# Performance work log

Hardware: AMD Instinct MI355X
Metric: run time of the kernel (lower is better)

The kernel has to match this reference:

```python
import jax, jax.numpy as jnp
import numpy as np

B, S, V, E, HID = 16, 40, 1004, 256, 256
C, R, HW = 1024, 256, 32  # featureChannel, releMapChannel, spatial
BN_EPS = 1e-5


def setup_inputs() -> dict:
    key = jax.random.key(0)
    ks = jax.random.split(key, 16)
    sc = 0.05
    emb = jax.random.normal(ks[4], (V, E), jnp.float32) * sc
    emb = emb.at[0].set(0.0)  # padding_idx = 0
    return {
        "feature": jax.random.normal(ks[0], (B, C, HW, HW), jnp.float32),
        "depth": jax.random.uniform(ks[1], (B, 1, HW, HW), jnp.float32),
        "instruction_idx": jax.random.randint(ks[2], (B, S), 0, V, jnp.int32),
        "instruction_length": jnp.clip(jax.random.randint(ks[3], (B,), 1, S + 1, jnp.int32), 1, S),
        "only_train_rele": 1,
        "emb_table": emb,
        "w_ih": jax.random.normal(ks[5], (4 * HID, E), jnp.float32) * sc,
        "w_hh": jax.random.normal(ks[6], (4 * HID, HID), jnp.float32) * sc,
        "b_ih": jax.random.normal(ks[7], (4 * HID,), jnp.float32) * sc,
        "b_hh": jax.random.normal(ks[8], (4 * HID,), jnp.float32) * sc,
        "e2d_w": jax.random.normal(ks[9], (HID, HID), jnp.float32) * sc,
        "e2d_b": jax.random.normal(ks[10], (HID,), jnp.float32) * sc,
        "lin1_w": jax.random.normal(ks[11], (R * C, HID), jnp.float32) * sc,
        "lin1_b": jax.random.normal(ks[12], (R * C,), jnp.float32) * sc,
        "bn_gamma": jnp.ones((R,), jnp.float32),
        "bn_beta": jnp.zeros((R,), jnp.float32),
        "bn_mean": jax.random.normal(ks[13], (R,), jnp.float32) * 0.01,
        "bn_var": jnp.ones((R,), jnp.float32),
    }


def _encoder_lstm(idx, lengths, emb_table, w_ih, w_hh, b_ih, b_hh, e2d_w, e2d_b):
    # Faithful to packed-sequence LSTM: state stops updating at each sample's length.
    embeds = emb_table[idx]                      # [B,S,E]
    xs = jnp.swapaxes(embeds, 0, 1)              # [S,B,E]
    mask = (jnp.arange(S)[:, None] < lengths[None, :])  # [S,B]
    h0 = jnp.zeros((B, HID), embeds.dtype)
    c0 = jnp.zeros((B, HID), embeds.dtype)

    def step(carry, xm):
        h, c = carry
        x_t, m = xm                              # [B,E], [B]
        gates = x_t @ w_ih.T + h @ w_hh.T + (b_ih + b_hh)  # [B,4H]
        i, f, g, o = jnp.split(gates, 4, axis=-1)  # torch gate order: i,f,g,o
        c_new = jax.nn.sigmoid(f) * c + jax.nn.sigmoid(i) * jnp.tanh(g)
        h_new = jax.nn.sigmoid(o) * jnp.tanh(c_new)
        m = m[:, None]
        return (jnp.where(m, h_new, h), jnp.where(m, c_new, c)), None

    (h_t, _), _ = jax.lax.scan(step, (h0, c0), (xs, mask))
    return jnp.tanh(h_t @ e2d_w.T + e2d_b)       # [B,HID]


def reference(feature, depth, instruction_idx, instruction_length, only_train_rele,
              emb_table, w_ih, w_hh, b_ih, b_hh, e2d_w, e2d_b,
              lin1_w, lin1_b, bn_gamma, bn_beta, bn_mean, bn_var):
    instr = _encoder_lstm(instruction_idx, instruction_length, emb_table,
                          w_ih, w_hh, b_ih, b_hh, e2d_w, e2d_b)  # [B,HID]
    # per-sample dynamic 1x1 filters (dropout in eval mode -> identity)
    f1 = jax.nn.leaky_relu(instr @ lin1_w.T + lin1_b, negative_slope=0.01)
    f1 = f1.reshape(B, R, C)
    # batched per-sample 1x1 conv: one einsum replaces the batch loop of F.conv2d
    rele = jax.nn.relu(jnp.einsum('bchw,brc->brhw', feature, f1))  # [B,R,H,W]
    # BatchNorm2d in eval mode with running stats
    scale = bn_gamma / jnp.sqrt(bn_var + BN_EPS)
    rele = rele * scale[None, :, None, None] + (bn_beta - bn_mean * scale)[None, :, None, None]
    single = jnp.max(rele, axis=1)               # channel-max pooling -> [B,H,W]
    return jnp.clip(single, 0.0, 1.0)
```

## Files before the change

kernel.cpp:

```cpp
#include <hip/hip_runtime.h>
#include <hip/hip_fp16.h>
#include <math.h>

#define NB 16
#define SQ 40
#define HIDN 256
#define CC 1024
#define NROW 262144

#define AGENT __HIP_MEMORY_SCOPE_AGENT
#define SENT 0x7E7E7E7Eu

__device__ __forceinline__ float sigf(float x){ return 1.0f/(1.0f+__expf(-x)); }

typedef _Float16 h2v __attribute__((ext_vector_type(2)));
typedef _Float16 f16x8 __attribute__((ext_vector_type(8)));
typedef float    f32x4 __attribute__((ext_vector_type(4)));

__device__ __forceinline__ float fd2(unsigned w, unsigned h, float acc){
  h2v a = __builtin_bit_cast(h2v, w);
  h2v b = __builtin_bit_cast(h2v, h);
#if __has_builtin(__builtin_amdgcn_fdot2)
  return __builtin_amdgcn_fdot2(a, b, acc, false);
#else
  return acc + (float)a.x*(float)b.x + (float)a.y*(float)b.y;
#endif
}

__device__ __forceinline__ unsigned pkh(float lo, float hi){
  return (unsigned)__half_as_ushort(__float2half_rn(lo))
       | ((unsigned)__half_as_ushort(__float2half_rn(hi)) << 16);
}

__global__ __launch_bounds__(256) void k_xgates(
    const int* __restrict__ idx, const float* __restrict__ emb,
    const float* __restrict__ w_ih, const float* __restrict__ b_ih,
    const float* __restrict__ b_hh, float* __restrict__ XG)
{
  __shared__ float xs[8*256];
  int t = threadIdx.x;
  int tb0 = blockIdx.x * 8;
  #pragma unroll
  for (int i = 0; i < 8; ++i) {
    int flat = t + i*256;
    int p = flat >> 8, k = flat & 255;
    int tb = tb0 + p;
    int ts = tb >> 4, b = tb & 15;
    int row = idx[b*SQ + ts];
    xs[p*256 + k] = emb[row*256 + k];
  }
  __syncthreads();
  int rows[4];
  float acc[4][8];
  #pragma unroll
  for (int r = 0; r < 4; ++r) {
    rows[r] = t + r*256;
    float bias = b_ih[rows[r]] + b_hh[rows[r]];
    #pragma unroll
    for (int p = 0; p < 8; ++p) acc[r][p] = bias;
  }
  for (int k16 = 0; k16 < 16; ++k16) {
    float4 w[4][4];
    #pragma unroll
    for (int r = 0; r < 4; ++r)
      #pragma unroll
      for (int q = 0; q < 4; ++q)
        w[r][q] = *(const float4*)&w_ih[rows[r]*256 + k16*16 + q*4];
    #pragma unroll
    for (int p = 0; p < 8; ++p) {
      #pragma unroll
      for (int q = 0; q < 4; ++q) {
        float4 x = *(const float4*)&xs[p*256 + k16*16 + q*4];
        #pragma unroll
        for (int r = 0; r < 4; ++r)
          acc[r][p] += w[r][q].x*x.x + w[r][q].y*x.y + w[r][q].z*x.z + w[r][q].w*x.w;
      }
    }
  }
  #pragma unroll
  for (int p = 0; p < 8; ++p)
    #pragma unroll
    for (int r = 0; r < 4; ++r)
      XG[(tb0 + p)*1024 + rows[r]] = acc[r][p];
}

__global__ __launch_bounds__(256) void k_whh3(const float* __restrict__ w, unsigned* __restrict__ W3)
{
  int tid = blockIdx.x*256 + threadIdx.x;
  int c    = tid & 3;
  int tt   = (tid >> 2) & 511;
  int q    = (tid >> 11) & 31;
  int half = tid >> 16;
  int pair = 4*q + c;
  int g = tt >> 7, j = tt & 127;
  int row = g*256 + half*128 + j;
  float2 v = *(const float2*)&w[(size_t)row*256 + 2*pair];
  W3[tid] = pkh(v.x, v.y);
}

__global__ __launch_bounds__(512) void k_lstm2(
    const float* __restrict__ XG, const uint4* __restrict__ W3,
    const int* __restrict__ lens, const float* __restrict__ e2d_w,
    const float* __restrict__ e2d_b, float* __restrict__ instr,
    unsigned* __restrict__ hcomm)
{
  __shared__ float dot_s[512];
  __shared__ float h_s[128];
  __shared__ float h_e[256];

  int t = threadIdx.x;
  int b    = blockIdx.x & 15;
  int half = blockIdx.x >> 4;
  int len  = lens[b];
  int lane = t & 63;

  unsigned wv[128];
  {
    const uint4* wp = W3 + (size_t)half*32*512 + t;
    #pragma unroll
    for (int q = 0; q < 32; ++q) {
      uint4 v = wp[(size_t)q*512];
      wv[4*q+0]=v.x; wv[4*q+1]=v.y; wv[4*q+2]=v.z; wv[4*q+3]=v.w;
    }
  }

  int g = t >> 7, j = t & 127;
  int row = g*256 + half*128 + j;
  float c_reg = 0.0f, h_reg = 0.0f;

  for (int it = 0; it < SQ; ++it) {
    float acc = XG[(it*NB + b)*1024 + row];
    if (it > 0) {
      unsigned own = pkh(h_s[2*lane], h_s[2*lane + 1]);
      int owni = (int)own;
      const unsigned* oslot = hcomm + ((it-1)*NB + b)*128 + (half ? 0 : 64);
      if (half == 0) {
        #pragma unroll
        for (int q = 0; q < 64; ++q)
          acc = fd2(wv[q], (unsigned)__builtin_amdgcn_readlane(owni, q), acc);
        unsigned oth;
        do { oth = __hip_atomic_load(oslot + lane, __ATOMIC_RELAXED, AGENT); }
        while (__any((int)(oth == SENT)));
        int othi = (int)oth;
        #pragma unroll
        for (int q = 0; q < 64; ++q)
          acc = fd2(wv[64+q], (unsigned)__builtin_amdgcn_readlane(othi, q), acc);
      } else {
        #pragma unroll
        for (int q = 0; q < 64; ++q)
          acc = fd2(wv[64+q], (unsigned)__builtin_amdgcn_readlane(owni, q), acc);
        unsigned oth;
        do { oth = __hip_atomic_load(oslot + lane, __ATOMIC_RELAXED, AGENT); }
        while (__any((int)(oth == SENT)));
        int othi = (int)oth;
        #pragma unroll
        for (int q = 0; q < 64; ++q)
          acc = fd2(wv[q], (unsigned)__builtin_amdgcn_readlane(othi, q), acc);
      }
    }
    dot_s[t] = acc;
    __syncthreads();
    if (t < 128) {
      float iv = sigf (dot_s[t]);
      float fv = sigf (dot_s[t + 128]);
      float gv = tanhf(dot_s[t + 256]);
      float ov = sigf (dot_s[t + 384]);
      float cn = fv*c_reg + iv*gv;
      float hn = ov*tanhf(cn);
      if (it < len) { c_reg = cn; h_reg = hn; }
      h_s[t] = h_reg;
    }
    __syncthreads();
    if (t < 64)
      __hip_atomic_store(hcomm + (it*NB + b)*128 + half*64 + t,
                         pkh(h_s[2*t], h_s[2*t+1]), __ATOMIC_RELAXED, AGENT);
  }

  if (half == 0) {
    const unsigned* slot = hcomm + ((SQ-1)*NB + b)*128;
    if (t < 64) {
      unsigned v0, v1;
      do {
        v0 = __hip_atomic_load(slot + t,      __ATOMIC_RELAXED, AGENT);
        v1 = __hip_atomic_load(slot + 64 + t, __ATOMIC_RELAXED, AGENT);
      } while (__any((int)(v0 == SENT)) || __any((int)(v1 == SENT)));
      h2v lo = __builtin_bit_cast(h2v, v0);
      h2v hi = __builtin_bit_cast(h2v, v1);
      h_e[2*t]       = (float)lo.x;  h_e[2*t + 1]       = (float)lo.y;
      h_e[128 + 2*t] = (float)hi.x;  h_e[128 + 2*t + 1] = (float)hi.y;
    }
    __syncthreads();
    if (t < 256) {
      float acc2 = e2d_b[t];
      const float4* wp2 = (const float4*)&e2d_w[t*256];
      #pragma unroll 8
      for (int k4 = 0; k4 < 64; ++k4) {
        float4 w = wp2[k4];
        float4 h4 = *(const float4*)&h_e[k4*4];
        acc2 += w.x*h4.x + w.y*h4.y + w.z*h4.z + w.w*h4.w;
      }
      instr[b*256 + t] = tanhf(acc2);
    }
  }
}

__global__ __launch_bounds__(256) void k_lin1(
    const float* __restrict__ instr, const float* __restrict__ w,
    const float* __restrict__ bias, _Float16* __restrict__ f1h)
{
  __shared__ float is[4096];
  int t = threadIdx.x;
  #pragma unroll
  for (int i = 0; i < 16; ++i) is[t + i*256] = instr[t + i*256];
  __syncthreads();
  int r0 = blockIdx.x*512 + t;
  int r1 = r0 + 256;
  const float* w0 = &w[(size_t)r0*256];
  const float* w1 = &w[(size_t)r1*256];
  float acc0[16], acc1[16];
  float bz0 = bias[r0], bz1 = bias[r1];
  #pragma unroll
  for (int i = 0; i < 16; ++i){ acc0[i]=bz0; acc1[i]=bz1; }
  for (int k16 = 0; k16 < 16; ++k16) {
    float4 a[4], bb[4];
    #pragma unroll
    for (int q = 0; q < 4; ++q){
      a[q]  = *(const float4*)&w0[k16*16 + q*4];
      bb[q] = *(const float4*)&w1[k16*16 + q*4];
    }
    #pragma unroll
    for (int bi = 0; bi < 16; ++bi) {
      #pragma unroll
      for (int q = 0; q < 4; ++q) {
        float4 x = *(const float4*)&is[bi*256 + k16*16 + q*4];
        acc0[bi] += a[q].x*x.x + a[q].y*x.y + a[q].z*x.z + a[q].w*x.w;
        acc1[bi] += bb[q].x*x.x + bb[q].y*x.y + bb[q].z*x.z + bb[q].w*x.w;
      }
    }
  }
  #pragma unroll
  for (int bi = 0; bi < 16; ++bi) {
    float v0 = acc0[bi]; v0 = v0 > 0.0f ? v0 : 0.01f*v0;
    float v1 = acc1[bi]; v1 = v1 > 0.0f ? v1 : 0.01f*v1;
    f1h[(size_t)bi*NROW + r0] = (_Float16)v0;
    f1h[(size_t)bi*NROW + r1] = (_Float16)v1;
  }
}

__global__ __launch_bounds__(256, 1) void k_einsum_mfma(
    const uint4* __restrict__ f1h4, const float* __restrict__ feat,
    const float* __restrict__ gamma, const float* __restrict__ beta,
    const float* __restrict__ mean, const float* __restrict__ var,
    float* __restrict__ out)
{
  __shared__ unsigned ALDS[256*20];
  __shared__ unsigned BLDS[128*20];
  __shared__ float sc_s[256], sh_s[256];
  __shared__ float red[2][128];

  int t = threadIdx.x;
  int b  = blockIdx.x >> 3;
  int P0 = (blockIdx.x & 7) * 128;
  int wid  = t >> 6, lane = t & 63;
  int wp = wid & 1, wr = wid >> 1;
  int col = lane & 15, quad = lane >> 4;

  {
    float s = gamma[t] * rsqrtf(var[t] + 1e-5f);
    sc_s[t] = s;
    sh_s[t] = beta[t] - mean[t]*s;
  }

  f32x4 acc[8][4];
  #pragma unroll
  for (int mt = 0; mt < 8; ++mt)
    #pragma unroll
    for (int nt = 0; nt < 4; ++nt) acc[mt][nt] = (f32x4)0.0f;

  const uint4* arow = f1h4 + ((size_t)b*NROW + (size_t)t*1024)/8;
  int p_loc = t & 127, khalf = t >> 7;
  const float* bbase = feat + ((size_t)b*1024 + khalf*16)*1024 + P0 + p_loc;

  uint4 apf[4];
  float bpf[16];
  #pragma unroll
  for (int g = 0; g < 4; ++g) apf[g] = arow[g];
  #pragma unroll
  for (int j = 0; j < 16; ++j) bpf[j] = bbase[(size_t)j*1024];

  for (int kc = 0; kc < 32; ++kc) {
    __syncthreads();
    #pragma unroll
    for (int g = 0; g < 4; ++g)
      *(uint4*)&ALDS[t*20 + g*4] = apf[g];
    {
      unsigned u[8];
      #pragma unroll
      for (int i = 0; i < 8; ++i) u[i] = pkh(bpf[2*i], bpf[2*i+1]);
      uint4 w0 = {u[0],u[1],u[2],u[3]}, w1 = {u[4],u[5],u[6],u[7]};
      *(uint4*)&BLDS[p_loc*20 + khalf*8]     = w0;
      *(uint4*)&BLDS[p_loc*20 + khalf*8 + 4] = w1;
    }
    __syncthreads();
    if (kc + 1 < 32) {
      #pragma unroll
      for (int g = 0; g < 4; ++g) apf[g] = arow[(kc+1)*4 + g];
      const float* bb = bbase + (size_t)(kc+1)*32*1024;
      #pragma unroll
      for (int j = 0; j < 16; ++j) bpf[j] = bb[(size_t)j*1024];
    }
    f16x8 bf[4];
    #pragma unroll
    for (int nt = 0; nt < 4; ++nt) {
      uint4 raw = *(const uint4*)&BLDS[(wp*64 + nt*16 + col)*20 + quad*4];
      bf[nt] = __builtin_bit_cast(f16x8, raw);
    }
    #pragma unroll
    for (int mt = 0; mt < 8; ++mt) {
      uint4 raw = *(const uint4*)&ALDS[(wr*128 + mt*16 + col)*20 + quad*4];
      f16x8 af = __builtin_bit_cast(f16x8, raw);
      #pragma unroll
      for (int nt = 0; nt < 4; ++nt)
        acc[mt][nt] = __builtin_amdgcn_mfma_f32_16x16x32_f16(af, bf[nt], acc[mt][nt], 0, 0, 0);
    }
  }

  float pmax[4];
  #pragma unroll
  for (int nt = 0; nt < 4; ++nt) pmax[nt] = -3.4e38f;
  #pragma unroll
  for (int mt = 0; mt < 8; ++mt) {
    int rb = wr*128 + mt*16 + quad*4;
    f32x4 scv = *(const f32x4*)&sc_s[rb];
    f32x4 shv = *(const f32x4*)&sh_s[rb];
    #pragma unroll
    for (int nt = 0; nt < 4; ++nt) {
      f32x4 a = acc[mt][nt];
      #pragma unroll
      for (int reg = 0; reg < 4; ++reg) {
        float v = fmaxf(a[reg], 0.0f)*scv[reg] + shv[reg];
        pmax[nt] = fmaxf(pmax[nt], v);
      }
    }
  }
  #pragma unroll
  for (int nt = 0; nt < 4; ++nt) {
    float m = pmax[nt];
    m = fmaxf(m, __shfl_xor(m, 16));
    m = fmaxf(m, __shfl_xor(m, 32));
    if (lane < 16) red[wr][wp*64 + nt*16 + lane] = m;
  }
  __syncthreads();
  if (t < 128) {
    float v = fmaxf(red[0][t], red[1][t]);
    out[b*1024 + P0 + t] = fminf(fmaxf(v, 0.0f), 1.0f);
  }
}

extern "C" void kernel_launch(void* const* d_in, const int* in_sizes, int n_in,
                              void* d_out, int out_size, void* d_ws, size_t ws_size,
                              hipStream_t stream)
{
  const float* feature = (const float*)d_in[0];
  const int*   idx     = (const int*)d_in[2];
  const int*   lens    = (const int*)d_in[3];
  const float* emb     = (const float*)d_in[5];
  const float* w_ih    = (const float*)d_in[6];
  const float* w_hh    = (const float*)d_in[7];
  const float* b_ih    = (const float*)d_in[8];
  const float* b_hh    = (const float*)d_in[9];
  const float* e2d_w   = (const float*)d_in[10];
  const float* e2d_b   = (const float*)d_in[11];
  const float* lin1_w  = (const float*)d_in[12];
  const float* lin1_b  = (const float*)d_in[13];
  const float* gamma   = (const float*)d_in[14];
  const float* beta    = (const float*)d_in[15];
  const float* mean    = (const float*)d_in[16];
  const float* var     = (const float*)d_in[17];

  char* ws = (char*)d_ws;
  float*    XG     = (float*)(ws);
  float*    instr  = (float*)(ws + 2621440);
  unsigned* W3     = (unsigned*)(ws + 2637824);
  unsigned* hcomm  = (unsigned*)(ws + 3162112);
  _Float16* f1h    = (_Float16*)(ws + 3489792);

  hipMemsetAsync(hcomm, 0x7E, 327680, stream);
  k_xgates <<<80,  256, 0, stream>>>(idx, emb, w_ih, b_ih, b_hh, XG);
  k_whh3   <<<512, 256, 0, stream>>>(w_hh, W3);
  k_lstm2  <<<32,  512, 0, stream>>>(XG, (const uint4*)W3, lens, e2d_w, e2d_b, instr, hcomm);
  k_lin1   <<<512, 256, 0, stream>>>(instr, lin1_w, lin1_b, f1h);
  k_einsum_mfma <<<128, 256, 0, stream>>>((const uint4*)f1h, feature, gamma, beta, mean, var,
                                          (float*)d_out);
}
```

Before: 614.7 us.

## Use one 1024-thread LSTM block per sample and double grid sizes of lin1/einsum

Replaces the two-block-per-sample LSTM, which exchanged hidden state through global atomics with spin-waits and a memset, with a single 1024-thread block per sample. Each thread now holds one full row of W_hh in fp16 registers, and the hidden state is shared through LDS. The next step's XG value is prefetched and the dot product is split into two accumulators to shorten the dependency chain. The lin1 kernel drops from two rows per thread to one, and the einsum tile shrinks from 128 to 64 pixels per block. Both grids double, giving more parallelism at the cost of more redundant A-tile loads in the einsum.

Result: slower. 1.184 ms (+92.6%).

```diff
diff --git a/kernel.cpp b/kernel.cpp
--- a/kernel.cpp
+++ b/kernel.cpp
@@ -7,9 +7,6 @@
 #define HIDN 256
 #define CC 1024
 #define NROW 262144
-
-#define AGENT __HIP_MEMORY_SCOPE_AGENT
-#define SENT 0x7E7E7E7Eu
 
 __device__ __forceinline__ float sigf(float x){ return 1.0f/(1.0f+__expf(-x)); }
 
@@ -84,123 +81,100 @@
       XG[(tb0 + p)*1024 + rows[r]] = acc[r][p];
 }
 
-__global__ __launch_bounds__(256) void k_whh3(const float* __restrict__ w, unsigned* __restrict__ W3)
+__global__ __launch_bounds__(256) void k_whh4(const float* __restrict__ w, uint4* __restrict__ W4)
 {
   int tid = blockIdx.x*256 + threadIdx.x;
-  int c    = tid & 3;
-  int tt   = (tid >> 2) & 511;
-  int q    = (tid >> 11) & 31;
-  int half = tid >> 16;
-  int pair = 4*q + c;
-  int g = tt >> 7, j = tt & 127;
-  int row = g*256 + half*128 + j;
-  float2 v = *(const float2*)&w[(size_t)row*256 + 2*pair];
-  W3[tid] = pkh(v.x, v.y);
-}
-
-__global__ __launch_bounds__(512) void k_lstm2(
-    const float* __restrict__ XG, const uint4* __restrict__ W3,
+  int row = tid >> 5;
+  int q4  = tid & 31;
+  const float* src = &w[(size_t)row*256 + q4*8];
+  float4 a = *(const float4*)src;
+  float4 b = *(const float4*)(src + 4);
+  uint4 o;
+  o.x = pkh(a.x, a.y);
+  o.y = pkh(a.z, a.w);
+  o.z = pkh(b.x, b.y);
+  o.w = pkh(b.z, b.w);
+  W4[(size_t)q4*1024 + row] = o;
+}
+
+__global__ __launch_bounds__(1024) void k_lstm1b(
+    const float* __restrict__ XG, const uint4* __restrict__ W4,
     const int* __restrict__ lens, const float* __restrict__ e2d_w,
-    const float* __restrict__ e2d_b, float* __restrict__ instr,
-    unsigned* __restrict__ hcomm)
-{
-  __shared__ float dot_s[512];
-  __shared__ float h_s[128];
-  __shared__ float h_e[256];
+    const float* __restrict__ e2d_b, float* __restrict__ instr)
+{
+  __shared__ float dot_s[1024];
+  __shared__ float h_s[256];
+  __shared__ unsigned h_pk[128];
 
   int t = threadIdx.x;
-  int b    = blockIdx.x & 15;
-  int half = blockIdx.x >> 4;
-  int len  = lens[b];
+  int b = blockIdx.x;
+  int len = lens[b];
   int lane = t & 63;
 
   unsigned wv[128];
+  #pragma unroll
+  for (int q4 = 0; q4 < 32; ++q4) {
+    uint4 v = W4[(size_t)q4*1024 + t];
+    wv[4*q4+0]=v.x; wv[4*q4+1]=v.y; wv[4*q4+2]=v.z; wv[4*q4+3]=v.w;
+  }
+
+  float c0 = 0.0f, c1 = 0.0f, h0r = 0.0f, h1r = 0.0f;
+
+  float xg_cur = XG[(0*NB + b)*1024 + t];
+
+  for (int it = 0; it < SQ; ++it) {
+    float xg_next = (it+1 < SQ) ? XG[((it+1)*NB + b)*1024 + t] : 0.0f;
+    float acc = xg_cur;
+    if (it > 0) {
+      int hp0 = (int)h_pk[lane];
+      int hp1 = (int)h_pk[64 + lane];
+      float a0 = acc, a1 = 0.0f;
+      #pragma unroll
+      for (int q = 0; q < 64; q += 2) {
+        a0 = fd2(wv[q],   (unsigned)__builtin_amdgcn_readlane(hp0, q),   a0);
+        a1 = fd2(wv[q+1], (unsigned)__builtin_amdgcn_readlane(hp0, q+1), a1);
+      }
+      #pragma unroll
+      for (int q = 0; q < 64; q += 2) {
+        a0 = fd2(wv[64+q],   (unsigned)__builtin_amdgcn_readlane(hp1, q),   a0);
+        a1 = fd2(wv[64+q+1], (unsigned)__builtin_amdgcn_readlane(hp1, q+1), a1);
+      }
+      acc = a0 + a1;
+    }
+    dot_s[t] = acc;
+    __syncthreads();
+    if (t < 128) {
+      float2 di = *(const float2*)&dot_s[2*t];
+      float2 df = *(const float2*)&dot_s[2*t + 256];
+      float2 dg = *(const float2*)&dot_s[2*t + 512];
+      float2 dv = *(const float2*)&dot_s[2*t + 768];
+      float cn0 = sigf(df.x)*c0 + sigf(di.x)*tanhf(dg.x);
+      float hn0 = sigf(dv.x)*tanhf(cn0);
+      float cn1 = sigf(df.y)*c1 + sigf(di.y)*tanhf(dg.y);
+      float hn1 = sigf(dv.y)*tanhf(cn1);
+      if (it < len) { c0 = cn0; h0r = hn0; c1 = cn1; h1r = hn1; }
+      h_pk[t] = pkh(h0r, h1r);
+      h_s[2*t] = h0r; h_s[2*t + 1] = h1r;
+    }
+    __syncthreads();
+    xg_cur = xg_next;
+  }
+
   {
-    const uint4* wp = W3 + (size_t)half*32*512 + t;
-    #pragma unroll
-    for (int q = 0; q < 32; ++q) {
-      uint4 v = wp[(size_t)q*512];
-      wv[4*q+0]=v.x; wv[4*q+1]=v.y; wv[4*q+2]=v.z; wv[4*q+3]=v.w;
-    }
-  }
-
-  int g = t >> 7, j = t & 127;
-  int row = g*256 + half*128 + j;
-  float c_reg = 0.0f, h_reg = 0.0f;
-
-  for (int it = 0; it < SQ; ++it) {
-    float acc = XG[(it*NB + b)*1024 + row];
-    if (it > 0) {
-      unsigned own = pkh(h_s[2*lane], h_s[2*lane + 1]);
-      int owni = (int)own;
-      const unsigned* oslot = hcomm + ((it-1)*NB + b)*128 + (half ? 0 : 64);
-      if (half == 0) {
-        #pragma unroll
-        for (int q = 0; q < 64; ++q)
-          acc = fd2(wv[q], (unsigned)__builtin_amdgcn_readlane(owni, q), acc);
-        unsigned oth;
-        do { oth = __hip_atomic_load(oslot + lane, __ATOMIC_RELAXED, AGENT); }
-        while (__any((int)(oth == SENT)));
-        int othi = (int)oth;
-        #pragma unroll
-        for (int q = 0; q < 64; ++q)
-          acc = fd2(wv[64+q], (unsigned)__builtin_amdgcn_readlane(othi, q), acc);
-      } else {
-        #pragma unroll
-        for (int q = 0; q < 64; ++q)
-          acc = fd2(wv[64+q], (unsigned)__builtin_amdgcn_readlane(owni, q), acc);
-        unsigned oth;
-        do { oth = __hip_atomic_load(oslot + lane, __ATOMIC_RELAXED, AGENT); }
-        while (__any((int)(oth == SENT)));
-        int othi = (int)oth;
-        #pragma unroll
-        for (int q = 0; q < 64; ++q)
-          acc = fd2(wv[q], (unsigned)__builtin_amdgcn_readlane(othi, q), acc);
-      }
-    }
-    dot_s[t] = acc;
-    __syncthreads();
-    if (t < 128) {
-      float iv = sigf (dot_s[t]);
-      float fv = sigf (dot_s[t + 128]);
-      float gv = tanhf(dot_s[t + 256]);
-      float ov = sigf (dot_s[t + 384]);
-      float cn = fv*c_reg + iv*gv;
-      float hn = ov*tanhf(cn);
-      if (it < len) { c_reg = cn; h_reg = hn; }
-      h_s[t] = h_reg;
-    }
-    __syncthreads();
-    if (t < 64)
-      __hip_atomic_store(hcomm + (it*NB + b)*128 + half*64 + t,
-                         pkh(h_s[2*t], h_s[2*t+1]), __ATOMIC_RELAXED, AGENT);
-  }
-
-  if (half == 0) {
-    const unsigned* slot = hcomm + ((SQ-1)*NB + b)*128;
-    if (t < 64) {
-      unsigned v0, v1;
-      do {
-        v0 = __hip_atomic_load(slot + t,      __ATOMIC_RELAXED, AGENT);
-        v1 = __hip_atomic_load(slot + 64 + t, __ATOMIC_RELAXED, AGENT);
-      } while (__any((int)(v0 == SENT)) || __any((int)(v1 == SENT)));
-      h2v lo = __builtin_bit_cast(h2v, v0);
-      h2v hi = __builtin_bit_cast(h2v, v1);
-      h_e[2*t]       = (float)lo.x;  h_e[2*t + 1]       = (float)lo.y;
-      h_e[128 + 2*t] = (float)hi.x;  h_e[128 + 2*t + 1] = (float)hi.y;
-    }
-    __syncthreads();
-    if (t < 256) {
-      float acc2 = e2d_b[t];
-      const float4* wp2 = (const float4*)&e2d_w[t*256];
-      #pragma unroll 8
-      for (int k4 = 0; k4 < 64; ++k4) {
-        float4 w = wp2[k4];
-        float4 h4 = *(const float4*)&h_e[k4*4];
-        acc2 += w.x*h4.x + w.y*h4.y + w.z*h4.z + w.w*h4.w;
-      }
-      instr[b*256 + t] = tanhf(acc2);
-    }
+    int r2 = t & 255, g2 = t >> 8;
+    float part = 0.0f;
+    const float4* wp2 = (const float4*)&e2d_w[(size_t)r2*256 + g2*64];
+    const float4* hp4 = (const float4*)&h_s[g2*64];
+    #pragma unroll
+    for (int k4 = 0; k4 < 16; ++k4) {
+      float4 w = wp2[k4];
+      float4 h4 = hp4[k4];
+      part += w.x*h4.x + w.y*h4.y + w.z*h4.z + w.w*h4.w;
+    }
+    dot_s[t] = part;
+    __syncthreads();
+    if (t < 256)
+      instr[b*256 + t] = tanhf(e2d_b[t] + dot_s[t] + dot_s[t+256] + dot_s[t+512] + dot_s[t+768]);
   }
 }
 
@@ -213,37 +187,30 @@
   #pragma unroll
   for (int i = 0; i < 16; ++i) is[t + i*256] = instr[t + i*256];
   __syncthreads();
-  int r0 = blockIdx.x*512 + t;
-  int r1 = r0 + 256;
+  int r0 = blockIdx.x*256 + t;
   const float* w0 = &w[(size_t)r0*256];
-  const float* w1 = &w[(size_t)r1*256];
-  float acc0[16], acc1[16];
-  float bz0 = bias[r0], bz1 = bias[r1];
-  #pragma unroll
-  for (int i = 0; i < 16; ++i){ acc0[i]=bz0; acc1[i]=bz1; }
+  float acc0[16];
+  float bz0 = bias[r0];
+  #pragma unroll
+  for (int i = 0; i < 16; ++i) acc0[i] = bz0;
   for (int k16 = 0; k16 < 16; ++k16) {
-    float4 a[4], bb[4];
-    #pragma unroll
-    for (int q = 0; q < 4; ++q){
-      a[q]  = *(const float4*)&w0[k16*16 + q*4];
-      bb[q] = *(const float4*)&w1[k16*16 + q*4];
-    }
+    float4 a[4];
+    #pragma unroll
+    for (int q = 0; q < 4; ++q)
+      a[q] = *(const float4*)&w0[k16*16 + q*4];
     #pragma unroll
     for (int bi = 0; bi < 16; ++bi) {
       #pragma unroll
       for (int q = 0; q < 4; ++q) {
         float4 x = *(const float4*)&is[bi*256 + k16*16 + q*4];
         acc0[bi] += a[q].x*x.x + a[q].y*x.y + a[q].z*x.z + a[q].w*x.w;
-        acc1[bi] += bb[q].x*x.x + bb[q].y*x.y + bb[q].z*x.z + bb[q].w*x.w;
       }
     }
   }
   #pragma unroll
   for (int bi = 0; bi < 16; ++bi) {
     float v0 = acc0[bi]; v0 = v0 > 0.0f ? v0 : 0.01f*v0;
-    float v1 = acc1[bi]; v1 = v1 > 0.0f ? v1 : 0.01f*v1;
     f1h[(size_t)bi*NROW + r0] = (_Float16)v0;
-    f1h[(size_t)bi*NROW + r1] = (_Float16)v1;
   }
 }
 
@@ -254,15 +221,14 @@
     float* __restrict__ out)
 {
   __shared__ unsigned ALDS[256*20];
-  __shared__ unsigned BLDS[128*20];
+  __shared__ unsigned BLDS[64*20];
   __shared__ float sc_s[256], sh_s[256];
-  __shared__ float red[2][128];
+  __shared__ float red[4][64];
 
   int t = threadIdx.x;
-  int b  = blockIdx.x >> 3;
-  int P0 = (blockIdx.x & 7) * 128;
-  int wid  = t >> 6, lane = t & 63;
-  int wp = wid & 1, wr = wid >> 1;
+  int b  = blockIdx.x >> 4;
+  int P0 = (blockIdx.x & 15) * 64;
+  int wr = t >> 6, lane = t & 63;
   int col = lane & 15, quad = lane >> 4;
 
   {
@@ -271,22 +237,22 @@
     sh_s[t] = beta[t] - mean[t]*s;
   }
 
-  f32x4 acc[8][4];
-  #pragma unroll
-  for (int mt = 0; mt < 8; ++mt)
+  f32x4 acc[4][4];
+  #pragma unroll
+  for (int mt = 0; mt < 4; ++mt)
     #pragma unroll
     for (int nt = 0; nt < 4; ++nt) acc[mt][nt] = (f32x4)0.0f;
 
   const uint4* arow = f1h4 + ((size_t)b*NROW + (size_t)t*1024)/8;
-  int p_loc = t & 127, khalf = t >> 7;
-  const float* bbase = feat + ((size_t)b*1024 + khalf*16)*1024 + P0 + p_loc;
+  int p_loc = t & 63, kq = t >> 6;
+  const float* bbase = feat + ((size_t)b*1024 + kq*8)*1024 + P0 + p_loc;
 
   uint4 apf[4];
-  float bpf[16];
+  float bpf[8];
   #pragma unroll
   for (int g = 0; g < 4; ++g) apf[g] = arow[g];
   #pragma unroll
-  for (int j = 0; j < 16; ++j) bpf[j] = bbase[(size_t)j*1024];
+  for (int j = 0; j < 8; ++j) bpf[j] = bbase[(size_t)j*1024];
 
   for (int kc = 0; kc < 32; ++kc) {
     __syncthreads();
@@ -294,12 +260,11 @@
     for (int g = 0; g < 4; ++g)
       *(uint4*)&ALDS[t*20 + g*4] = apf[g];
     {
-      unsigned u[8];
-      #pragma unroll
-      for (int i = 0; i < 8; ++i) u[i] = pkh(bpf[2*i], bpf[2*i+1]);
-      uint4 w0 = {u[0],u[1],u[2],u[3]}, w1 = {u[4],u[5],u[6],u[7]};
-      *(uint4*)&BLDS[p_loc*20 + khalf*8]     = w0;
-      *(uint4*)&BLDS[p_loc*20 + khalf*8 + 4] = w1;
+      unsigned u[4];
+      #pragma unroll
+      for (int c = 0; c < 4; ++c) u[c] = pkh(bpf[2*c], bpf[2*c+1]);
+      uint4 w0 = {u[0],u[1],u[2],u[3]};
+      *(uint4*)&BLDS[p_loc*20 + kq*4] = w0;
     }
     __syncthreads();
     if (kc + 1 < 32) {
@@ -307,17 +272,17 @@
       for (int g = 0; g < 4; ++g) apf[g] = arow[(kc+1)*4 + g];
       const float* bb = bbase + (size_t)(kc+1)*32*1024;
       #pragma unroll
-      for (int j = 0; j < 16; ++j) bpf[j] = bb[(size_t)j*1024];
+      for (int j = 0; j < 8; ++j) bpf[j] = bb[(size_t)j*1024];
     }
     f16x8 bf[4];
     #pragma unroll
     for (int nt = 0; nt < 4; ++nt) {
-      uint4 raw = *(const uint4*)&BLDS[(wp*64 + nt*16 + col)*20 + quad*4];
+      uint4 raw = *(const uint4*)&BLDS[(nt*16 + col)*20 + quad*4];
       bf[nt] = __builtin_bit_cast(f16x8, raw);
     }
     #pragma unroll
-    for (int mt = 0; mt < 8; ++mt) {
-      uint4 raw = *(const uint4*)&ALDS[(wr*128 + mt*16 + col)*20 + quad*4];
+    for (int mt = 0; mt < 4; ++mt) {
+      uint4 raw = *(const uint4*)&ALDS[(wr*64 + mt*16 + col)*20 + quad*4];
       f16x8 af = __builtin_bit_cast(f16x8, raw);
       #pragma unroll
       for (int nt = 0; nt < 4; ++nt)
@@ -329,8 +294,8 @@
   #pragma unroll
   for (int nt = 0; nt < 4; ++nt) pmax[nt] = -3.4e38f;
   #pragma unroll
-  for (int mt = 0; mt < 8; ++mt) {
-    int rb = wr*128 + mt*16 + quad*4;
+  for (int mt = 0; mt < 4; ++mt) {
+    int rb = wr*64 + mt*16 + quad*4;
     f32x4 scv = *(const f32x4*)&sc_s[rb];
     f32x4 shv = *(const f32x4*)&sh_s[rb];
     #pragma unroll
@@ -348,11 +313,11 @@
     float m = pmax[nt];
     m = fmaxf(m, __shfl_xor(m, 16));
     m = fmaxf(m, __shfl_xor(m, 32));
-    if (lane < 16) red[wr][wp*64 + nt*16 + lane] = m;
+    if (lane < 16) red[wr][nt*16 + lane] = m;
   }
   __syncthreads();
-  if (t < 128) {
-    float v = fmaxf(red[0][t], red[1][t]);
+  if (t < 64) {
+    float v = fmaxf(fmaxf(red[0][t], red[1][t]), fmaxf(red[2][t], red[3][t]));
     out[b*1024 + P0 + t] = fminf(fmaxf(v, 0.0f), 1.0f);
   }
 }
@@ -381,15 +346,13 @@
   char* ws = (char*)d_ws;
   float*    XG     = (float*)(ws);
   float*    instr  = (float*)(ws + 2621440);
-  unsigned* W3     = (unsigned*)(ws + 2637824);
-  unsigned* hcomm  = (unsigned*)(ws + 3162112);
-  _Float16* f1h    = (_Float16*)(ws + 3489792);
-
-  hipMemsetAsync(hcomm, 0x7E, 327680, stream);
-  k_xgates <<<80,  256, 0, stream>>>(idx, emb, w_ih, b_ih, b_hh, XG);
-  k_whh3   <<<512, 256, 0, stream>>>(w_hh, W3);
-  k_lstm2  <<<32,  512, 0, stream>>>(XG, (const uint4*)W3, lens, e2d_w, e2d_b, instr, hcomm);
-  k_lin1   <<<512, 256, 0, stream>>>(instr, lin1_w, lin1_b, f1h);
-  k_einsum_mfma <<<128, 256, 0, stream>>>((const uint4*)f1h, feature, gamma, beta, mean, var,
+  uint4*    W4     = (uint4*)(ws + 2637824);
+  _Float16* f1h    = (_Float16*)(ws + 3162112);
+
+  k_xgates <<<80,   256,  0, stream>>>(idx, emb, w_ih, b_ih, b_hh, XG);
+  k_whh4   <<<128,  256,  0, stream>>>(w_hh, W4);
+  k_lstm1b <<<16,   1024, 0, stream>>>(XG, W4, lens, e2d_w, e2d_b, instr);
+  k_lin1   <<<1024, 256,  0, stream>>>(instr, lin1_w, lin1_b, f1h);
+  k_einsum_mfma <<<256, 256, 0, stream>>>((const uint4*)f1h, feature, gamma, beta, mean, var,
                                           (float*)d_out);
 }
```
